# Kernel tuning notes

Hardware: AMD Instinct MI355X
Metric: run time of the kernel (lower is better)

The kernel has to match this reference:

```python
import jax, jax.numpy as jnp
import numpy as np

B, S, D = 4, 2048, 1024


def setup_inputs() -> dict:
    key = jax.random.key(0)
    kq, k1, k2, k3 = jax.random.split(key, 4)
    w_scale = 1.0 / np.sqrt(D)  # ~ glorot scale for square Dense
    q = jax.random.normal(kq, (B, S, D), dtype=jnp.float32)
    Wq = jax.random.normal(k1, (D, D), dtype=jnp.float32) * w_scale
    Wk = jax.random.normal(k2, (D, D), dtype=jnp.float32) * w_scale  # unused in self-attn path (bug in original)
    Wv = jax.random.normal(k3, (D, D), dtype=jnp.float32) * w_scale
    # causal mask: 1 = masked (future), matching tf.where(mask == 1, -1e9, scores)
    mask = jnp.triu(jnp.ones((S, S), dtype=jnp.int32), k=1)
    return {"q": q, "Wq": Wq, "Wk": Wk, "Wv": Wv, "mask": mask}


def reference(q, Wq, Wk, Wv, mask):
    # Self-attention path of the original: k=None, v=None.
    WQ = jnp.einsum('bsd,de->bse', q, Wq)
    # Faithful to the original code: dense_v is applied for BOTH K and V.
    WKV = jnp.einsum('bsd,de->bse', q, Wv)
    d_k = jnp.asarray(D, dtype=q.dtype)
    scores = jnp.einsum('bqd,bkd->bqk', WQ, WKV) / jnp.sqrt(d_k)  # [B,S,S]
    scores = jnp.where(mask == 1, jnp.asarray(-1e9, scores.dtype), scores)
    attn = jax.nn.softmax(scores, axis=-1)
    return jnp.einsum('bqk,bkd->bqd', attn, WKV)
```

## Files before the change

### kernel.cpp

```cpp
#include <hip/hip_runtime.h>


typedef unsigned short u16;
typedef short short8 __attribute__((ext_vector_type(8)));
typedef float floatx4 __attribute__((ext_vector_type(4)));

#define S_LEN 2048
#define D_DIM 1024
#define BK 64

__device__ inline u16 f2b(float f) {
  unsigned u = __float_as_uint(f);
  return (u16)((u + 0x7fffu + ((u >> 16) & 1u)) >> 16);
}

__device__ __forceinline__ void gload16(const u16* g, u16* l) {
  __builtin_amdgcn_global_load_lds(
      (const __attribute__((address_space(1))) void*)g,
      (__attribute__((address_space(3))) void*)l, 16, 0, 0);
}

__global__ __launch_bounds__(256)
void cvt_f32_bf16(const float* __restrict__ src, u16* __restrict__ dst) {
  size_t idx = ((size_t)blockIdx.x * 256 + threadIdx.x) * 8;
  float4 a0 = *(const float4*)&src[idx];
  float4 a1 = *(const float4*)&src[idx + 4];
  short8 v;
  v[0] = (short)f2b(a0.x); v[1] = (short)f2b(a0.y);
  v[2] = (short)f2b(a0.z); v[3] = (short)f2b(a0.w);
  v[4] = (short)f2b(a1.x); v[5] = (short)f2b(a1.y);
  v[6] = (short)f2b(a1.z); v[7] = (short)f2b(a1.w);
  *(short8*)&dst[idx] = v;
}

__global__ __launch_bounds__(256)
void transpose_cvt2(const float* __restrict__ s0, u16* __restrict__ d0_,
                    const float* __restrict__ s1, u16* __restrict__ d1_) {
  __shared__ u16 tile[32][33];
  const float* src = blockIdx.z ? s1 : s0;
  u16* dst = blockIdx.z ? d1_ : d0_;
  int c0 = blockIdx.x * 32, r0 = blockIdx.y * 32;
  int tx = threadIdx.x, ty = threadIdx.y;
  for (int ii = 0; ii < 32; ii += 8)
    tile[ii + ty][tx] = f2b(src[(size_t)(r0 + ii + ty) * 1024 + (c0 + tx)]);
  __syncthreads();
  for (int ii = 0; ii < 32; ii += 8)
    dst[(size_t)(c0 + ii + ty) * 1024 + (r0 + tx)] = tile[tx][ii + ty];
}

__global__ __launch_bounds__(512)
void gemm_proj(const u16* __restrict__ A, const u16* __restrict__ B0,
               const u16* __restrict__ B1, u16* __restrict__ C0,
               u16* __restrict__ C1, u16* __restrict__ WKVt) {
  __shared__ __align__(16) u16 lds[65536];

  int id = blockIdx.x;
  int xcd = id & 7, i5 = id >> 3;
  int m_idx = xcd * 4 + (i5 & 3);
  int n_idx = i5 >> 2;
  int z = n_idx >> 2;
  int n0 = (n_idx & 3) * 256;
  int m0 = m_idx * 256;
  const u16* Bp = z ? B1 : B0;
  u16* Cp = z ? C1 : C0;

  int tid = threadIdx.x;
  int wv = tid >> 6, lane = tid & 63, quad = lane >> 4, l15 = lane & 15;
  int wm = wv >> 2, wn = wv & 3;

  int off_g[2];
#pragma unroll
  for (int l = 0; l < 2; ++l) {
    int chunk = (wv * 2 + l) * 64 + lane;
    int r = chunk >> 3, cs = chunk & 7;
    off_g[l] = r * 1024 + (cs ^ (r & 7)) * 8;
  }
  const u16* As0 = A + (size_t)m0 * 1024;
  const u16* As1 = A + (size_t)(m0 + 128) * 1024;
  const u16* Bs0 = Bp + (size_t)n0 * 1024;
  const u16* Bs1 = Bp + (size_t)(n0 + 128) * 1024;

#define PSTAGE(src, reg)                                                     \
  {                                                                          \
    _Pragma("unroll") for (int l = 0; l < 2; ++l)                            \
        gload16((src) + off_g[l], &lds[(reg) * 8192 + (wv * 2 + l) * 512]);  \
  }

  int aoff[2], boff[2];
#pragma unroll
  for (int kk = 0; kk < 2; ++kk) {
    int c = ((kk * 4 + quad) ^ (l15 & 7)) * 8;
    aoff[kk] = l15 * 64 + c;
    boff[kk] = ((wn & 1) * 64 + l15) * 64 + c;
  }
  const u16* A0p = &lds[(0 + wm) * 8192];
  const u16* A1p = &lds[(4 + wm) * 8192];
  const u16* B0p = &lds[(2 + (wn >> 1)) * 8192];
  const u16* B1p = &lds[(6 + (wn >> 1)) * 8192];

  floatx4 acc[8][4];
#pragma unroll
  for (int i = 0; i < 8; ++i)
#pragma unroll
    for (int j = 0; j < 4; ++j) acc[i][j] = (floatx4){0.f, 0.f, 0.f, 0.f};

#define BARp() __builtin_amdgcn_s_barrier()
#define WLG() asm volatile("s_waitcnt lgkmcnt(0)" ::: "memory")
#define WVM(n) asm volatile("s_waitcnt vmcnt(" #n ")" ::: "memory")

#define RDA(dst, base, fb)                                                 \
  _Pragma("unroll") for (int f = 0; f < 4; ++f)                            \
  _Pragma("unroll") for (int kk = 0; kk < 2; ++kk)                         \
      dst[f][kk] = *(const short8*)&(base)[((fb) + f) * 1024 + aoff[kk]];
#define RDB(dst, base, fb)                                                 \
  _Pragma("unroll") for (int f = 0; f < 2; ++f)                            \
  _Pragma("unroll") for (int kk = 0; kk < 2; ++kk)                         \
      dst[f][kk] = *(const short8*)&(base)[((fb) + f) * 1024 + boff[kk]];
#define MMQ(mh, nh, afq, bfq)                                              \
  __builtin_amdgcn_s_setprio(1);                                           \
  _Pragma("unroll") for (int f = 0; f < 4; ++f)                            \
  _Pragma("unroll") for (int g2 = 0; g2 < 2; ++g2)                         \
  _Pragma("unroll") for (int kk = 0; kk < 2; ++kk)                         \
      acc[(mh) * 4 + f][(nh) * 2 + g2] =                                   \
          __builtin_amdgcn_mfma_f32_16x16x32_bf16(                         \
              afq[f][kk], bfq[g2][kk], acc[(mh) * 4 + f][(nh) * 2 + g2],   \
              0, 0, 0);                                                    \
  __builtin_amdgcn_s_setprio(0);

  PSTAGE(As0, 0); PSTAGE(As1, 1); PSTAGE(Bs0, 2); PSTAGE(Bs1, 3);
  PSTAGE(As0 + 64, 4); PSTAGE(As1 + 64, 5);
  WVM(4);
  BARp();

#pragma unroll 1
  for (int it = 0; it < 8; ++it) {
    int kb = it * 128;
    short8 af0[4][2], af1[4][2], bf0[2][2], bf1[2][2];
    RDA(af0, A0p, 0); RDB(bf0, B0p, 0);
    PSTAGE(Bs0 + kb + 64, 6);
    BARp(); WLG();
    MMQ(0, 0, af0, bf0);
    BARp();
    RDA(af1, A0p, 4); RDB(bf1, B0p, 2);
    PSTAGE(Bs1 + kb + 64, 7);
    BARp(); WLG();
    MMQ(1, 1, af1, bf1);
    BARp();
    if (it < 7) PSTAGE(As0 + kb + 128, 0);
    BARp();
    MMQ(0, 1, af0, bf1);
    BARp();
    if (it < 7) PSTAGE(As1 + kb + 128, 1);
    BARp();
    MMQ(1, 0, af1, bf0);
    if (it < 7) { WVM(4); } else { WVM(0); }
    BARp();
    RDA(af0, A1p, 0); RDB(bf0, B1p, 0);
    if (it < 7) PSTAGE(Bs0 + kb + 128, 2);
    BARp(); WLG();
    MMQ(0, 0, af0, bf0);
    BARp();
    RDA(af1, A1p, 4); RDB(bf1, B1p, 2);
    if (it < 7) PSTAGE(Bs1 + kb + 128, 3);
    BARp(); WLG();
    MMQ(1, 1, af1, bf1);
    BARp();
    if (it < 7) PSTAGE(As0 + kb + 192, 4);
    BARp();
    MMQ(0, 1, af0, bf1);
    BARp();
    if (it < 7) PSTAGE(As1 + kb + 192, 5);
    BARp();
    MMQ(1, 0, af1, bf0);
    if (it < 7) WVM(4);
    BARp();
  }

  asm volatile("s_waitcnt vmcnt(0) lgkmcnt(0)" ::: "memory");
#pragma unroll
  for (int mf = 0; mf < 8; ++mf)
#pragma unroll
    for (int nf = 0; nf < 4; ++nf)
#pragma unroll
      for (int r = 0; r < 4; ++r)
        Cp[(size_t)(m0 + wm * 128 + mf * 16 + quad * 4 + r) * D_DIM +
           (n0 + wn * 64 + nf * 16 + l15)] = f2b(acc[mf][nf][r]);

  if (z) {
    int b = m0 >> 11, srow = m0 & 2047;
    u16* Wt = WKVt + (size_t)b * D_DIM * S_LEN;
#pragma unroll
    for (int ph = 0; ph < 2; ++ph) {
      BARp();
      if ((wn >> 1) == ph) {
#pragma unroll
        for (int mf = 0; mf < 8; ++mf)
#pragma unroll
          for (int nf = 0; nf < 4; ++nf)
#pragma unroll
            for (int r = 0; r < 4; ++r)
              lds[((wn & 1) * 64 + nf * 16 + l15) * 272 +
                  (wm * 128 + mf * 16 + quad * 4 + r)] = f2b(acc[mf][nf][r]);
      }
      BARp();
#pragma unroll
      for (int rr = 0; rr < 8; ++rr) {
        int idx = rr * 512 + tid;
        int dl = idx >> 5, sc = idx & 31;
        *(short8*)&Wt[(size_t)(n0 + ph * 128 + dl) * S_LEN + srow + sc * 8] =
            *(const short8*)&lds[dl * 272 + sc * 8];
      }
    }
  }
}

#define GEMM64_PROLOG()                                                       \
  __shared__ u16 Als[64 * BK];                                                \
  __shared__ u16 Bls[128 * BK];                                               \
  int tid = threadIdx.x;                                                      \
  int wave = tid >> 6, lane = tid & 63, quad = lane >> 4, l15 = lane & 15;    \
  int wr = (wave >> 1) * 32, wc = (wave & 1) * 64;                            \
  int arow = lane >> 3;                                                       \
  int acol = ((lane & 7) ^ (arow & 7)) << 3;                                  \
  floatx4 acc[2][4];                                                          \
  _Pragma("unroll") for (int i = 0; i < 2; ++i)                               \
  _Pragma("unroll") for (int j = 0; j < 4; ++j)                               \
      acc[i][j] = (floatx4){0.f, 0.f, 0.f, 0.f};

#define GEMM64_KLOOP(Aptr, lda, Bptr, ldb, KEND)                              \
  for (int kb = 0; kb < (KEND); kb += BK) {                                   \
    __syncthreads();                                                          \
    _Pragma("unroll") for (int p = 0; p < 2; ++p) {                           \
      int r0 = wave * 16 + p * 8;                                             \
      gload16(&(Aptr)[(size_t)(m0 + r0 + arow) * (lda) + kb + acol],          \
              &Als[r0 * BK]);                                                 \
    }                                                                         \
    _Pragma("unroll") for (int p = 0; p < 4; ++p) {                           \
      int r0 = wave * 32 + p * 8;                                             \
      gload16(&(Bptr)[(size_t)(n0 + r0 + arow) * (ldb) + kb + acol],          \
              &Bls[r0 * BK]);                                                 \
    }                                                                         \
    __syncthreads();                                                          \
    _Pragma("unroll") for (int kk8 = 0; kk8 < 8; kk8 += 4) {                  \
      int cg = (((kk8 + quad) & 7) ^ (l15 & 7)) << 3;                         \
      short8 af[2], bfr[4];                                                   \
      _Pragma("unroll") for (int i = 0; i < 2; ++i)                           \
          af[i] = *(const short8*)&Als[(wr + i * 16 + l15) * BK + cg];        \
      _Pragma("unroll") for (int j = 0; j < 4; ++j)                           \
          bfr[j] = *(const short8*)&Bls[(wc + j * 16 + l15) * BK + cg];       \
      _Pragma("unroll") for (int i = 0; i < 2; ++i)                           \
      _Pragma("unroll") for (int j = 0; j < 4; ++j)                           \
          acc[i][j] = __builtin_amdgcn_mfma_f32_16x16x32_bf16(                \
              af[i], bfr[j], acc[i][j], 0, 0, 0);                             \
    }                                                                         \
  }

__global__ __launch_bounds__(256)
void gemm_scores(const u16* __restrict__ WQ, const u16* __restrict__ WKV,
                 u16* __restrict__ Pp, float* __restrict__ rowsum) {
  int id = blockIdx.x;
  int xcd = id & 7;
  int b = xcd & 3, h = xcd >> 2;
  int t = id >> 3;
  int m = (int)((sqrtf(8.f * (float)t + 1.f) - 1.f) * 0.5f);
  while ((m + 1) * (m + 2) / 2 <= t) ++m;
  while (m * (m + 1) / 2 > t) --m;
  int bj = t - m * (m + 1) / 2;
  int bi = 2 * m + h;
  int m0 = bi * 64, n0 = bj * 128;
  const u16* A = WQ + (size_t)b * S_LEN * D_DIM;
  const u16* Bp = WKV + (size_t)b * S_LEN * D_DIM;
  GEMM64_PROLOG();
  GEMM64_KLOOP(A, D_DIM, Bp, D_DIM, D_DIM);
  u16* Pb = Pp + (size_t)b * S_LEN * S_LEN;
  float part[2][4];
#pragma unroll
  for (int i = 0; i < 2; ++i)
#pragma unroll
    for (int r = 0; r < 4; ++r) part[i][r] = 0.f;
#pragma unroll
  for (int i = 0; i < 2; ++i)
#pragma unroll
    for (int j = 0; j < 4; ++j) {
      int col = n0 + wc + j * 16 + l15;
#pragma unroll
      for (int r = 0; r < 4; ++r) {
        int row = m0 + wr + i * 16 + quad * 4 + r;
        float p = (col > row) ? 0.f : __expf(acc[i][j][r] * 0.03125f);
        Pb[(size_t)row * S_LEN + col] = f2b(p);
        part[i][r] += p;
      }
    }
#pragma unroll
  for (int i = 0; i < 2; ++i)
#pragma unroll
    for (int r = 0; r < 4; ++r) {
      float v = part[i][r];
#pragma unroll
      for (int off = 1; off < 16; off <<= 1) v += __shfl_xor(v, off, 64);
      part[i][r] = v;
    }
  if (l15 == 0) {
#pragma unroll
    for (int i = 0; i < 2; ++i)
#pragma unroll
      for (int r = 0; r < 4; ++r)
        atomicAdd(&rowsum[b * S_LEN + m0 + wr + i * 16 + quad * 4 + r],
                  part[i][r]);
  }
}

__global__ __launch_bounds__(256)
void gemm_pv(const u16* __restrict__ Pp, const u16* __restrict__ WKVt,
             const float* __restrict__ rowsum, float* __restrict__ out) {
  int id = blockIdx.x;
  int xcd = id & 7;
  int b = xcd & 3, h = xcd >> 2;
  int r_ = id >> 3;
  int mh = 15 - (r_ >> 3);
  int bi = 2 * mh + h;
  int bj = r_ & 7;
  int m0 = bi * 64, n0 = bj * 128;
  int kend = (bi + 1) * 64;
  const u16* A = Pp + (size_t)b * S_LEN * S_LEN;
  const u16* Bp = WKVt + (size_t)b * (size_t)D_DIM * S_LEN;
  GEMM64_PROLOG();
  GEMM64_KLOOP(A, S_LEN, Bp, S_LEN, kend);
  const float* rs = rowsum + b * S_LEN;
  float* Co = out + (size_t)b * S_LEN * D_DIM;
#pragma unroll
  for (int i = 0; i < 2; ++i)
#pragma unroll
    for (int r = 0; r < 4; ++r) {
      int row = m0 + wr + i * 16 + quad * 4 + r;
      float inv = 1.0f / rs[row];
#pragma unroll
      for (int j = 0; j < 4; ++j)
        Co[(size_t)row * D_DIM + (n0 + wc + j * 16 + l15)] =
            acc[i][j][r] * inv;
    }
}

extern "C" void kernel_launch(void* const* d_in, const int* in_sizes, int n_in,
                              void* d_out, int out_size, void* d_ws, size_t ws_size,
                              hipStream_t stream) {
  const float* q = (const float*)d_in[0];
  const float* Wq = (const float*)d_in[1];
  const float* Wv = (const float*)d_in[3];
  char* ws = (char*)d_ws;
  const size_t MB = 1024 * 1024;
  u16* Wqt = (u16*)(ws);
  u16* Wvt = (u16*)(ws + 2 * MB);
  u16* qb16 = (u16*)(ws + 4 * MB);
  u16* Pp = (u16*)(ws);
  u16* WQ = (u16*)(ws + 32 * MB);
  u16* WKV = (u16*)(ws + 48 * MB);
  u16* WKVt = (u16*)(ws + 64 * MB);
  float* rowsum = (float*)(ws + 80 * MB);

  hipMemsetAsync(rowsum, 0, 4 * S_LEN * sizeof(float), stream);
  cvt_f32_bf16<<<4096, 256, 0, stream>>>(q, qb16);
  transpose_cvt2<<<dim3(32, 32, 2), dim3(32, 8), 0, stream>>>(Wq, Wqt, Wv, Wvt);
  gemm_proj<<<256, 512, 0, stream>>>(qb16, Wqt, Wvt, WQ, WKV, WKVt);
  gemm_scores<<<1088, 256, 0, stream>>>(WQ, WKV, Pp, rowsum);
  gemm_pv<<<1024, 256, 0, stream>>>(Pp, WKVt, rowsum, (float*)d_out);
}
```

Baseline: 232.0 us.

## Reorder projection GEMM pipeline to cut fragment registers and target two blocks per CU

```diff
diff --git a/kernel.cpp b/kernel.cpp
--- a/kernel.cpp
+++ b/kernel.cpp
@@ -48,7 +48,7 @@
     dst[(size_t)(c0 + ii + ty) * 1024 + (r0 + tx)] = tile[tx][ii + ty];
 }
 
-__global__ __launch_bounds__(512)
+__global__ __launch_bounds__(512, 2)
 void gemm_proj(const u16* __restrict__ A, const u16* __restrict__ B0,
                const u16* __restrict__ B1, u16* __restrict__ C0,
                u16* __restrict__ C1, u16* __restrict__ WKVt) {
@@ -128,51 +128,53 @@
   __builtin_amdgcn_s_setprio(0);
 
   PSTAGE(As0, 0); PSTAGE(As1, 1); PSTAGE(Bs0, 2); PSTAGE(Bs1, 3);
-  PSTAGE(As0 + 64, 4); PSTAGE(As1 + 64, 5);
-  WVM(4);
+  PSTAGE(As0 + 64, 4); PSTAGE(As1 + 64, 5); PSTAGE(Bs0 + 64, 6);
+  PSTAGE(Bs1 + 64, 7);
+  WVM(8);
   BARp();
 
 #pragma unroll 1
   for (int it = 0; it < 8; ++it) {
-    int kb = it * 128;
-    short8 af0[4][2], af1[4][2], bf0[2][2], bf1[2][2];
-    RDA(af0, A0p, 0); RDB(bf0, B0p, 0);
-    PSTAGE(Bs0 + kb + 64, 6);
-    BARp(); WLG();
-    MMQ(0, 0, af0, bf0);
-    BARp();
-    RDA(af1, A0p, 4); RDB(bf1, B0p, 2);
-    PSTAGE(Bs1 + kb + 64, 7);
-    BARp(); WLG();
-    MMQ(1, 1, af1, bf1);
-    BARp();
-    if (it < 7) PSTAGE(As0 + kb + 128, 0);
-    BARp();
-    MMQ(0, 1, af0, bf1);
-    BARp();
-    if (it < 7) PSTAGE(As1 + kb + 128, 1);
-    BARp();
-    MMQ(1, 0, af1, bf0);
-    if (it < 7) { WVM(4); } else { WVM(0); }
-    BARp();
-    RDA(af0, A1p, 0); RDB(bf0, B1p, 0);
-    if (it < 7) PSTAGE(Bs0 + kb + 128, 2);
-    BARp(); WLG();
-    MMQ(0, 0, af0, bf0);
-    BARp();
-    RDA(af1, A1p, 4); RDB(bf1, B1p, 2);
-    if (it < 7) PSTAGE(Bs1 + kb + 128, 3);
-    BARp(); WLG();
-    MMQ(1, 1, af1, bf1);
-    BARp();
-    if (it < 7) PSTAGE(As0 + kb + 192, 4);
-    BARp();
-    MMQ(0, 1, af0, bf1);
-    BARp();
-    if (it < 7) PSTAGE(As1 + kb + 192, 5);
-    BARp();
-    MMQ(1, 0, af1, bf0);
-    if (it < 7) WVM(4);
+    int kb2 = it * 128 + 128, kb3 = it * 128 + 192;
+    short8 af[4][2], bf0[2][2], bf1[2][2];
+    RDA(af, A0p, 0); RDB(bf0, B0p, 0);
+    BARp(); WLG();
+    MMQ(0, 0, af, bf0);
+    BARp();
+    RDB(bf1, B0p, 2);
+    BARp(); WLG();
+    MMQ(0, 1, af, bf1);
+    BARp();
+    RDA(af, A0p, 4);
+    if (it < 7) PSTAGE(Bs0 + kb2, 2);
+    BARp(); WLG();
+    MMQ(1, 1, af, bf1);
+    BARp();
+    if (it < 7) { PSTAGE(Bs1 + kb2, 3); PSTAGE(As0 + kb2, 0); }
+    BARp();
+    MMQ(1, 0, af, bf0);
+    if (it < 7) { WVM(6); } else { WVM(0); }
+    BARp();
+    RDA(af, A1p, 0); RDB(bf0, B1p, 0);
+    if (it < 7) PSTAGE(As1 + kb2, 1);
+    BARp(); WLG();
+    MMQ(0, 0, af, bf0);
+    BARp();
+    RDB(bf1, B1p, 2);
+    BARp(); WLG();
+    MMQ(0, 1, af, bf1);
+    BARp();
+    RDA(af, A1p, 4);
+    if (it < 7) PSTAGE(Bs0 + kb3, 6);
+    BARp(); WLG();
+    MMQ(1, 1, af, bf1);
+    BARp();
+    if (it < 7) {
+      PSTAGE(Bs1 + kb3, 7); PSTAGE(As0 + kb3, 4); PSTAGE(As1 + kb3, 5);
+    }
+    BARp();
+    MMQ(1, 0, af, bf0);
+    if (it < 7) WVM(8);
     BARp();
   }
 
```

Result: faster. 209.7 us (-9.6%).
